# Kernel tuning notes

Hardware: AMD Instinct MI355X
Metric: run time of the kernel (lower is better)

The kernel has to match this reference:

```python
import jax, jax.numpy as jnp
import numpy as np

N_NODES = 100000
N_EDGES = 1600000
IN_C, HID_C, OUT_C = 128, 128, 64


def gcn_conv(x, src, dst, W, b, num_nodes):
    # PyG GCNConv: add self-loops, symmetric normalization, linear transform,
    # aggregate source features into targets.
    h = x @ W  # [N, C_out]
    loop = jnp.arange(num_nodes, dtype=src.dtype)
    s = jnp.concatenate([src, loop])
    d = jnp.concatenate([dst, loop])
    deg = jax.ops.segment_sum(jnp.ones_like(d, dtype=h.dtype), d, num_segments=num_nodes)
    inv_sqrt = jnp.where(deg > 0, jax.lax.rsqrt(deg), 0.0)
    norm = inv_sqrt[s] * inv_sqrt[d]  # [E+N]
    msgs = h[s] * norm[:, None]  # gather + scale
    out = jax.ops.segment_sum(msgs, d, num_segments=num_nodes)  # scatter-add
    return out + b


def setup_inputs() -> dict:
    key = jax.random.key(0)
    k1, k2, k3, k4 = jax.random.split(key, 4)
    x = jax.random.normal(k1, (N_NODES, IN_C), dtype=jnp.float32)
    edge_index = jax.random.randint(k2, (2, N_EDGES), 0, N_NODES, dtype=jnp.int64)
    W1 = jax.random.normal(k3, (IN_C, HID_C), dtype=jnp.float32) * (1.0 / np.sqrt(IN_C))
    b1 = jnp.zeros((HID_C,), dtype=jnp.float32)
    W2 = jax.random.normal(k4, (HID_C, OUT_C), dtype=jnp.float32) * (1.0 / np.sqrt(HID_C))
    b2 = jnp.zeros((OUT_C,), dtype=jnp.float32)
    return {"x": x, "edge_index": edge_index, "W1": W1, "b1": b1, "W2": W2, "b2": b2}


def reference(x, edge_index, W1, b1, W2, b2):
    num_nodes = x.shape[0]
    src, dst = edge_index[0], edge_index[1]  # PyG flow: source -> target
    h = gcn_conv(x, src, dst, W1, b1, num_nodes)
    h = jax.nn.relu(h)  # dropout is identity in eval mode
    out = gcn_conv(h, src, dst, W2, b2, num_nodes)
    return out
```

## Files before the change

kernel.cpp:

```cpp
#include <hip/hip_runtime.h>

#define IN_C 128
#define HID_C 128
#define OUT_C 64

#define BSPAN 256
#define BCAP  5120
#define NBMAX 512
#define ACHUNK 4096

typedef unsigned int uint32;
typedef unsigned short ushort16;
typedef _Float16 f16;
typedef f16   f16x8 __attribute__((ext_vector_type(8)));
typedef float f32x4 __attribute__((ext_vector_type(4)));


__device__ __forceinline__ ushort16 f2bf(float f) {
    union { float f; uint32 u; } v; v.f = f;
    uint32 r = v.u + 0x7FFFu + ((v.u >> 16) & 1u);
    return (ushort16)(r >> 16);
}

__device__ __forceinline__ void unpack2(uint32 u, float& f0, float& f1) {
    union { uint32 x; float f; } a, b;
    a.x = u << 16;
    b.x = u & 0xFFFF0000u;
    f0 = a.f; f1 = b.f;
}

__device__ __forceinline__ void acc_row(uint4 r, float* acc) {
    float f0, f1;
    unpack2(r.x, f0, f1); acc[0] += f0; acc[1] += f1;
    unpack2(r.y, f0, f1); acc[2] += f0; acc[3] += f1;
    unpack2(r.z, f0, f1); acc[4] += f0; acc[5] += f1;
    unpack2(r.w, f0, f1); acc[6] += f0; acc[7] += f1;
}


__launch_bounds__(256)
__global__ void bin_edges_kernel(const int* __restrict__ src, const int* __restrict__ dst,
                                 int* __restrict__ bucketCur, uint32* __restrict__ binned,
                                 int E, int nbuck) {
    __shared__ int hist[NBMAX];
    __shared__ int base[NBMAX];
    const int tid = threadIdx.x;
    const int e0  = blockIdx.x * ACHUNK;

    for (int i = tid; i < NBMAX; i += 256) hist[i] = 0;
    __syncthreads();

    int d[16], s[16], rk[16];
#pragma unroll
    for (int j = 0; j < 16; j++) {
        int e = e0 + j * 256 + tid;
        if (e < E) {
            d[j] = dst[e];
            s[j] = src[e];
            rk[j] = atomicAdd(&hist[d[j] >> 8], 1);
        } else d[j] = -1;
    }
    __syncthreads();

    for (int b = tid; b < nbuck; b += 256) {
        int h = hist[b];
        base[b] = h ? atomicAdd(&bucketCur[b], h) : 0;
    }
    __syncthreads();

#pragma unroll
    for (int j = 0; j < 16; j++) {
        if (d[j] >= 0) {
            int b = d[j] >> 8;
            int pos = base[b] + rk[j];
            if (pos < BCAP)
                binned[(size_t)b * BCAP + pos] =
                    ((uint32)(d[j] & 255) << 17) | (uint32)s[j];
        }
    }
}


__launch_bounds__(256)
__global__ void bucket_csr_kernel(const uint32* __restrict__ binned,
                                  const int* __restrict__ bucketCur,
                                  int* __restrict__ csr_src, int* __restrict__ rowbeg,
                                  int* __restrict__ rowend, float* __restrict__ inv, int N) {
    constexpr int MAXIT = BCAP / 256;
    __shared__ int cnt[BSPAN];
    __shared__ int scn[BSPAN];
    __shared__ int excl[BSPAN];
    const int b   = blockIdx.x;
    const int tid = threadIdx.x;
    const int n0  = b * BSPAN;
    const int ne  = min(bucketCur[b], BCAP);
    const uint32* bp = binned + (size_t)b * BCAP;

    cnt[tid] = 0;
    __syncthreads();

    uint32 ebuf[MAXIT];
    int    rbuf[MAXIT];
    int nmine = 0;
    for (int i = tid; i < ne; i += 256) {
        uint32 e = bp[i];
        ebuf[nmine] = e;
        rbuf[nmine] = atomicAdd(&cnt[e >> 17], 1);
        nmine++;
    }
    __syncthreads();

    int v = cnt[tid];
    scn[tid] = v;
    __syncthreads();
    for (int off = 1; off < 256; off <<= 1) {
        int u = (tid >= off) ? scn[tid - off] : 0;
        __syncthreads();
        scn[tid] += u;
        __syncthreads();
    }
    int ex = scn[tid] - v;
    excl[tid] = ex;

    int n = n0 + tid;
    if (n < N) {
        int gb = b * BCAP + ex;
        rowbeg[n] = gb;
        rowend[n] = gb + v;
        inv[n] = rsqrtf((float)(v + 1));
    }
    __syncthreads();

    for (int j = 0; j < nmine; j++) {
        uint32 e = ebuf[j];
        csr_src[(size_t)b * BCAP + excl[e >> 17] + rbuf[j]] = (int)(e & 0x1FFFFu);
    }
}


template <int C>
__device__ __forceinline__ void wprep_one(const float* __restrict__ W, f16* __restrict__ Wf, int t) {
    constexpr int NCT = C / 16;
    int lane = t & 63;
    int ctkc = t >> 6;
    int ct = ctkc % NCT, kc = ctkc / NCT;
    int kbase = kc * 32 + (lane >> 4) * 8;
    int col   = ct * 16 + (lane & 15);
    f16 v[8];
#pragma unroll
    for (int j = 0; j < 8; j++) v[j] = (f16)W[(size_t)(kbase + j) * C + col];
    *(uint4*)(Wf + (size_t)t * 8) = *(const uint4*)v;
}

__global__ void wprep_both(const float* __restrict__ W1, f16* __restrict__ Wf1,
                           const float* __restrict__ W2, f16* __restrict__ Wf2,
                           int* __restrict__ bucketCur, int nbuck) {
    constexpr int T1 = 4 * (HID_C / 16) * 64;
    constexpr int T2 = 4 * (OUT_C / 16) * 64;
    int t = blockIdx.x * 256 + threadIdx.x;
    if (t < nbuck) bucketCur[t] = 0;
    if (t < T1)            wprep_one<HID_C>(W1, Wf1, t);
    else if (t < T1 + T2)  wprep_one<OUT_C>(W2, Wf2, t - T1);
}


template <int C>
__launch_bounds__(256)
__global__ void mfma_gemm(const float* __restrict__ X, const f16* __restrict__ Wf,
                          const float* __restrict__ inv, ushort16* __restrict__ outb, int N) {
    constexpr int NCT = C / 16;
    __shared__ __align__(16) f16 As[4 * 4 * 64 * 8];
    __shared__ __align__(16) f16 Bs[4 * NCT * 64 * 8];

    const int tid  = threadIdx.x;
    const int lane = tid & 63;
    const int w    = tid >> 6;
    const int row0 = blockIdx.x * 64;

    {
        constexpr int TOT = 4 * NCT * 64 * 8;
        const uint4* src = (const uint4*)Wf;
        uint4* dst = (uint4*)Bs;
#pragma unroll
        for (int i = 0; i < TOT / 8 / 256; i++)
            dst[tid + i * 256] = src[tid + i * 256];
    }

    {
        int r   = tid >> 2;
        int seg = tid & 3;
        int row = row0 + r;
        int ws_ = r >> 4;
        int r15 = r & 15;
#pragma unroll
        for (int i = 0; i < 8; i++) {
            int k = seg * 32 + i * 4;
            float4 v = make_float4(0.f, 0.f, 0.f, 0.f);
            if (row < N) v = *(const float4*)(X + (size_t)row * 128 + k);
            int q = (k >> 3) & 3, j0 = k & 7;
            f16 h[4] = {(f16)v.x, (f16)v.y, (f16)v.z, (f16)v.w};
            int slot = ((seg * 4 + ws_) * 64 + (q * 16 + r15)) * 8 + j0;
            *(uint2*)(As + slot) = *(const uint2*)h;
        }
    }
    __syncthreads();

    f32x4 acc[NCT];
#pragma unroll
    for (int c = 0; c < NCT; c++) acc[c] = (f32x4){0.f, 0.f, 0.f, 0.f};
#pragma unroll
    for (int kc = 0; kc < 4; kc++) {
        f16x8 a = *(const f16x8*)&As[((kc * 4 + w) * 64 + lane) * 8];
#pragma unroll
        for (int ct = 0; ct < NCT; ct++) {
            f16x8 b = *(const f16x8*)&Bs[((kc * NCT + ct) * 64 + lane) * 8];
            acc[ct] = __builtin_amdgcn_mfma_f32_16x16x32_f16(a, b, acc[ct], 0, 0, 0);
        }
    }

    __syncthreads();
    ushort16* Ds = (ushort16*)As;
    const int q = lane >> 4;
    float iv[4];
#pragma unroll
    for (int reg = 0; reg < 4; reg++) {
        int row = row0 + w * 16 + q * 4 + reg;
        iv[reg] = (row < N) ? inv[row] : 0.f;
    }
#pragma unroll
    for (int ct = 0; ct < NCT; ct++) {
#pragma unroll
        for (int reg = 0; reg < 4; reg++) {
            int r = w * 16 + q * 4 + reg;
            Ds[r * C + ct * 16 + (lane & 15)] = f2bf(acc[ct][reg] * iv[reg]);
        }
    }
    __syncthreads();
    {
        int r  = tid >> 2;
        int row = row0 + r;
        if (row < N) {
            constexpr int SPT = C / 4;
            int c0 = (tid & 3) * SPT;
            const uint4* s = (const uint4*)&Ds[r * C + c0];
            uint4* d = (uint4*)(outb + (size_t)row * C + c0);
#pragma unroll
            for (int i = 0; i < SPT / 8; i++) d[i] = s[i];
        }
    }
}


__launch_bounds__(512, 4)
__global__ void fused_gather_gemm(const int* __restrict__ rowbeg, const int* __restrict__ rowend,
                                  const int* __restrict__ csr,
                                  const ushort16* __restrict__ hsb,
                                  const float* __restrict__ inv, const float* __restrict__ bias1,
                                  const f16* __restrict__ Wf2,
                                  ushort16* __restrict__ outb, int N) {
    constexpr int CIN = 128, COUT = 64, NCT = COUT / 16;
    __shared__ __align__(16) f16 As[4 * 4 * 64 * 8];
    __shared__ __align__(16) f16 Bs[4 * NCT * 64 * 8];

    const int tid  = threadIdx.x;
    const int lane = tid & 63;
    const int w    = tid >> 6;
    const int row0 = blockIdx.x * 64;

    {
        const uint4* s = (const uint4*)Wf2;
        uint4* d = (uint4*)Bs;
        d[tid]       = s[tid];
        d[tid + 512] = s[tid + 512];
    }

    {
        const int r = tid >> 3;
        const int q = tid & 7;
        const int n = row0 + r;
        float acc[16];
#pragma unroll
        for (int j = 0; j < 16; j++) acc[j] = 0.f;

        if (n < N) {
            {
                const ushort16* base = hsb + (size_t)n * CIN + q * 16;
                uint4 s0 = *(const uint4*)(base);
                uint4 s1 = *(const uint4*)(base + 8);
                acc_row(s0, acc); acc_row(s1, acc + 8);
            }
            const int end = rowend[n];
            int i = rowbeg[n];
            for (; i + 4 <= end; i += 4) {
                const ushort16* p0 = hsb + (size_t)csr[i]     * CIN + q * 16;
                const ushort16* p1 = hsb + (size_t)csr[i + 1] * CIN + q * 16;
                const ushort16* p2 = hsb + (size_t)csr[i + 2] * CIN + q * 16;
                const ushort16* p3 = hsb + (size_t)csr[i + 3] * CIN + q * 16;
                uint4 a0 = *(const uint4*)(p0);
                uint4 a1 = *(const uint4*)(p0 + 8);
                uint4 b0 = *(const uint4*)(p1);
                uint4 b1 = *(const uint4*)(p1 + 8);
                uint4 c0 = *(const uint4*)(p2);
                uint4 c1 = *(const uint4*)(p2 + 8);
                uint4 d0 = *(const uint4*)(p3);
                uint4 d1 = *(const uint4*)(p3 + 8);
                acc_row(a0, acc); acc_row(a1, acc + 8);
                acc_row(b0, acc); acc_row(b1, acc + 8);
                acc_row(c0, acc); acc_row(c1, acc + 8);
                acc_row(d0, acc); acc_row(d1, acc + 8);
            }
            for (; i < end; i++) {
                const ushort16* p0 = hsb + (size_t)csr[i] * CIN + q * 16;
                uint4 a0 = *(const uint4*)(p0);
                uint4 a1 = *(const uint4*)(p0 + 8);
                acc_row(a0, acc); acc_row(a1, acc + 8);
            }

            float iv = inv[n];
#pragma unroll
            for (int j = 0; j < 16; j++)
                acc[j] = fmaxf(fmaf(iv, acc[j], bias1[q * 16 + j]), 0.f);
        }

        const int ws_ = r >> 4, r15 = r & 15;
        const int seg = q >> 1;
#pragma unroll
        for (int u = 0; u < 2; u++) {
            const int i8 = (q & 1) * 2 + u;
            f16 hv[8];
#pragma unroll
            for (int j = 0; j < 8; j++) hv[j] = (f16)acc[u * 8 + j];
            int slot = ((seg * 4 + ws_) * 64 + (i8 * 16 + r15)) * 8;
            *(uint4*)(As + slot) = *(const uint4*)hv;
        }
    }
    __syncthreads();

    f32x4 acc2[NCT];
#pragma unroll
    for (int c = 0; c < NCT; c++) acc2[c] = (f32x4){0.f, 0.f, 0.f, 0.f};
    if (w < 4) {
#pragma unroll
        for (int kc = 0; kc < 4; kc++) {
            f16x8 a = *(const f16x8*)&As[((kc * 4 + w) * 64 + lane) * 8];
#pragma unroll
            for (int ct = 0; ct < NCT; ct++) {
                f16x8 b = *(const f16x8*)&Bs[((kc * NCT + ct) * 64 + lane) * 8];
                acc2[ct] = __builtin_amdgcn_mfma_f32_16x16x32_f16(a, b, acc2[ct], 0, 0, 0);
            }
        }
    }

    __syncthreads();
    ushort16* Ds = (ushort16*)As;
    if (w < 4) {
        const int q2 = lane >> 4;
        float iv2[4];
#pragma unroll
        for (int reg = 0; reg < 4; reg++) {
            int row = row0 + w * 16 + q2 * 4 + reg;
            iv2[reg] = (row < N) ? inv[row] : 0.f;
        }
#pragma unroll
        for (int ct = 0; ct < NCT; ct++) {
#pragma unroll
            for (int reg = 0; reg < 4; reg++) {
                int r = w * 16 + q2 * 4 + reg;
                Ds[r * COUT + ct * 16 + (lane & 15)] = f2bf(acc2[ct][reg] * iv2[reg]);
            }
        }
    }
    __syncthreads();
    {
        const int r   = tid >> 3;
        const int row = row0 + r;
        if (row < N) {
            const int c0 = (tid & 7) * 8;
            *(uint4*)(outb + (size_t)row * COUT + c0) = *(const uint4*)&Ds[r * COUT + c0];
        }
    }
}


template <int C, bool RELU>
__launch_bounds__(256, 4)
__global__ void gather_agg_bf16(const int* __restrict__ rowbeg, const int* __restrict__ rowend,
                                const int* __restrict__ csr_src,
                                const ushort16* __restrict__ hsb, const float* __restrict__ inv,
                                const float* __restrict__ b, float* __restrict__ out, int N) {
    constexpr int TPN = 4;
    constexpr int CPT = C / TPN;
    constexpr int NPB = 256 / TPN;
    int n    = blockIdx.x * NPB + threadIdx.x / TPN;
    int lane = threadIdx.x % TPN;
    if (n >= N) return;
    const size_t c0 = (size_t)lane * CPT;

    float acc[16];
#pragma unroll
    for (int j = 0; j < 16; j++) acc[j] = 0.f;
    {
        const uint4* p = (const uint4*)(hsb + (size_t)n * C + c0);
        uint4 s0 = p[0], s1 = p[1];
        acc_row(s0, acc); acc_row(s1, acc + 8);
    }

    const int end = rowend[n];
    int i = rowbeg[n];
    for (; i + 4 <= end; i += 4) {
        const uint4* p0 = (const uint4*)(hsb + (size_t)csr_src[i]     * C + c0);
        const uint4* p1 = (const uint4*)(hsb + (size_t)csr_src[i + 1] * C + c0);
        const uint4* p2 = (const uint4*)(hsb + (size_t)csr_src[i + 2] * C + c0);
        const uint4* p3 = (const uint4*)(hsb + (size_t)csr_src[i + 3] * C + c0);
        uint4 a0 = p0[0], a1 = p0[1];
        uint4 b0 = p1[0], b1 = p1[1];
        uint4 cc0 = p2[0], cc1 = p2[1];
        uint4 d0 = p3[0], d1 = p3[1];
        acc_row(a0, acc);  acc_row(a1, acc + 8);
        acc_row(b0, acc);  acc_row(b1, acc + 8);
        acc_row(cc0, acc); acc_row(cc1, acc + 8);
        acc_row(d0, acc);  acc_row(d1, acc + 8);
    }
    for (; i < end; i++) {
        const uint4* p0 = (const uint4*)(hsb + (size_t)csr_src[i] * C + c0);
        uint4 a0 = p0[0], a1 = p0[1];
        acc_row(a0, acc); acc_row(a1, acc + 8);
    }

    float iv = inv[n];
    float r[16];
#pragma unroll
    for (int u = 0; u < 4; u++) {
        float4 bv = *(const float4*)(b + c0 + u * 4);
        r[u * 4 + 0] = fmaf(iv, acc[u * 4 + 0], bv.x);
        r[u * 4 + 1] = fmaf(iv, acc[u * 4 + 1], bv.y);
        r[u * 4 + 2] = fmaf(iv, acc[u * 4 + 2], bv.z);
        r[u * 4 + 3] = fmaf(iv, acc[u * 4 + 3], bv.w);
    }
    if (RELU) {
#pragma unroll
        for (int j = 0; j < 16; j++) r[j] = fmaxf(r[j], 0.f);
    }
    float* po = out + (size_t)n * C + c0;
#pragma unroll
    for (int u = 0; u < 4; u++)
        *(float4*)(po + u * 4) = make_float4(r[u * 4 + 0], r[u * 4 + 1], r[u * 4 + 2], r[u * 4 + 3]);
}

extern "C" void kernel_launch(void* const* d_in, const int* in_sizes, int n_in,
                              void* d_out, int out_size, void* d_ws, size_t ws_size,
                              hipStream_t stream) {
    const float* x  = (const float*)d_in[0];
    const int*   ei = (const int*)d_in[1];
    const float* W1 = (const float*)d_in[2];
    const float* b1 = (const float*)d_in[3];
    const float* W2 = (const float*)d_in[4];
    const float* b2 = (const float*)d_in[5];
    float* out = (float*)d_out;

    const int N = in_sizes[0] / IN_C;
    const int E = in_sizes[1] / 2;
    const int* src = ei;
    const int* dst = ei + E;
    const int nbuck = (N + BSPAN - 1) / BSPAN;

    char* ws = (char*)d_ws;
    auto align_up = [](size_t v) { return (v + 1023) & ~(size_t)1023; };
    size_t off = 0;
    int*      bucketCur = (int*)(ws + off);      off += align_up((size_t)nbuck * sizeof(int));
    float*    inv       = (float*)(ws + off);    off += align_up((size_t)N * sizeof(float));
    int*      rowbeg    = (int*)(ws + off);      off += align_up((size_t)N * sizeof(int));
    int*      rowend    = (int*)(ws + off);      off += align_up((size_t)N * sizeof(int));
    uint32*   binned    = (uint32*)(ws + off);   off += align_up((size_t)nbuck * BCAP * sizeof(uint32));
    int*      csrs      = (int*)(ws + off);      off += align_up((size_t)nbuck * BCAP * sizeof(int));
    f16*      Wf1       = (f16*)(ws + off);      off += align_up((size_t)4 * (HID_C/16) * 64 * 8 * sizeof(f16));
    f16*      Wf2       = (f16*)(ws + off);      off += align_up((size_t)4 * (OUT_C/16) * 64 * 8 * sizeof(f16));
    ushort16* hs1b      = (ushort16*)(ws + off); off += align_up((size_t)N * HID_C * sizeof(ushort16));
    ushort16* hs2b      = (ushort16*)(ws + off); off += align_up((size_t)N * OUT_C * sizeof(ushort16));

    wprep_both<<<(4 * (HID_C/16 + OUT_C/16) * 64 + 255) / 256, 256, 0, stream>>>(
        W1, Wf1, W2, Wf2, bucketCur, nbuck);
    bin_edges_kernel<<<(E + ACHUNK - 1) / ACHUNK, 256, 0, stream>>>(
        src, dst, bucketCur, binned, E, nbuck);
    bucket_csr_kernel<<<nbuck, 256, 0, stream>>>(
        binned, bucketCur, csrs, rowbeg, rowend, inv, N);

    mfma_gemm<HID_C><<<(N + 63) / 64, 256, 0, stream>>>(x, Wf1, inv, hs1b, N);

    fused_gather_gemm<<<(N + 63) / 64, 512, 0, stream>>>(
        rowbeg, rowend, csrs, hs1b, inv, b1, Wf2, hs2b, N);

    gather_agg_bf16<OUT_C, false><<<(N + 63) / 64, 256, 0, stream>>>(
        rowbeg, rowend, csrs, hs2b, inv, b2, out, N);
}
```

Measured before the change: 263.2 us.

## Store layer-2 features as fp16 column slices and gather per slice

```diff
diff --git a/kernel.cpp b/kernel.cpp
--- a/kernel.cpp
+++ b/kernel.cpp
@@ -257,7 +257,7 @@
                                   const ushort16* __restrict__ hsb,
                                   const float* __restrict__ inv, const float* __restrict__ bias1,
                                   const f16* __restrict__ Wf2,
-                                  ushort16* __restrict__ outb, int N) {
+                                  f16* __restrict__ hs2s, int N) {
     constexpr int CIN = 128, COUT = 64, NCT = COUT / 16;
     __shared__ __align__(16) f16 As[4 * 4 * 64 * 8];
     __shared__ __align__(16) f16 Bs[4 * NCT * 64 * 8];
@@ -352,7 +352,7 @@
     }
 
     __syncthreads();
-    ushort16* Ds = (ushort16*)As;
+    f16* Ds = (f16*)As;
     if (w < 4) {
         const int q2 = lane >> 4;
         float iv2[4];
@@ -366,7 +366,7 @@
 #pragma unroll
             for (int reg = 0; reg < 4; reg++) {
                 int r = w * 16 + q2 * 4 + reg;
-                Ds[r * COUT + ct * 16 + (lane & 15)] = f2bf(acc2[ct][reg] * iv2[reg]);
+                Ds[r * COUT + ct * 16 + (lane & 15)] = (f16)(acc2[ct][reg] * iv2[reg]);
             }
         }
     }
@@ -375,76 +375,67 @@
         const int r   = tid >> 3;
         const int row = row0 + r;
         if (row < N) {
-            const int c0 = (tid & 7) * 8;
-            *(uint4*)(outb + (size_t)row * COUT + c0) = *(const uint4*)&Ds[r * COUT + c0];
-        }
-    }
-}
-
-
-template <int C, bool RELU>
-__launch_bounds__(256, 4)
-__global__ void gather_agg_bf16(const int* __restrict__ rowbeg, const int* __restrict__ rowend,
-                                const int* __restrict__ csr_src,
-                                const ushort16* __restrict__ hsb, const float* __restrict__ inv,
-                                const float* __restrict__ b, float* __restrict__ out, int N) {
-    constexpr int TPN = 4;
-    constexpr int CPT = C / TPN;
-    constexpr int NPB = 256 / TPN;
-    int n    = blockIdx.x * NPB + threadIdx.x / TPN;
-    int lane = threadIdx.x % TPN;
+            const int c = tid & 7;
+            const int s = c >> 1, h = c & 1;
+            uint4 v = *(const uint4*)&Ds[r * COUT + c * 8];
+            *(uint4*)(hs2s + ((size_t)s * N + row) * 16 + h * 8) = v;
+        }
+    }
+}
+
+
+__launch_bounds__(256)
+__global__ void slice_gather2(const int* __restrict__ rowbeg, const int* __restrict__ rowend,
+                              const int* __restrict__ csr_src,
+                              const f16* __restrict__ hs2s,
+                              const float* __restrict__ inv, const float* __restrict__ b,
+                              float* __restrict__ out, int N) {
+    const int s = blockIdx.x & 3;
+    const int n = (blockIdx.x >> 2) * 256 + threadIdx.x;
     if (n >= N) return;
-    const size_t c0 = (size_t)lane * CPT;
+    const f16* base = hs2s + (size_t)s * N * 16;
 
     float acc[16];
-#pragma unroll
-    for (int j = 0; j < 16; j++) acc[j] = 0.f;
-    {
-        const uint4* p = (const uint4*)(hsb + (size_t)n * C + c0);
-        uint4 s0 = p[0], s1 = p[1];
-        acc_row(s0, acc); acc_row(s1, acc + 8);
+    {
+        const f16x8* p = (const f16x8*)(base + (size_t)n * 16);
+        f16x8 a0 = p[0], a1 = p[1];
+#pragma unroll
+        for (int j = 0; j < 8; j++) { acc[j] = (float)a0[j]; acc[8 + j] = (float)a1[j]; }
     }
 
     const int end = rowend[n];
     int i = rowbeg[n];
     for (; i + 4 <= end; i += 4) {
-        const uint4* p0 = (const uint4*)(hsb + (size_t)csr_src[i]     * C + c0);
-        const uint4* p1 = (const uint4*)(hsb + (size_t)csr_src[i + 1] * C + c0);
-        const uint4* p2 = (const uint4*)(hsb + (size_t)csr_src[i + 2] * C + c0);
-        const uint4* p3 = (const uint4*)(hsb + (size_t)csr_src[i + 3] * C + c0);
-        uint4 a0 = p0[0], a1 = p0[1];
-        uint4 b0 = p1[0], b1 = p1[1];
-        uint4 cc0 = p2[0], cc1 = p2[1];
-        uint4 d0 = p3[0], d1 = p3[1];
-        acc_row(a0, acc);  acc_row(a1, acc + 8);
-        acc_row(b0, acc);  acc_row(b1, acc + 8);
-        acc_row(cc0, acc); acc_row(cc1, acc + 8);
-        acc_row(d0, acc);  acc_row(d1, acc + 8);
+        const f16x8* p0 = (const f16x8*)(base + (size_t)csr_src[i]     * 16);
+        const f16x8* p1 = (const f16x8*)(base + (size_t)csr_src[i + 1] * 16);
+        const f16x8* p2 = (const f16x8*)(base + (size_t)csr_src[i + 2] * 16);
+        const f16x8* p3 = (const f16x8*)(base + (size_t)csr_src[i + 3] * 16);
+        f16x8 a0 = p0[0], a1 = p0[1];
+        f16x8 b0 = p1[0], b1 = p1[1];
+        f16x8 c0 = p2[0], c1 = p2[1];
+        f16x8 d0 = p3[0], d1 = p3[1];
+#pragma unroll
+        for (int j = 0; j < 8; j++) {
+            acc[j]     += (float)a0[j] + (float)b0[j] + (float)c0[j] + (float)d0[j];
+            acc[8 + j] += (float)a1[j] + (float)b1[j] + (float)c1[j] + (float)d1[j];
+        }
     }
     for (; i < end; i++) {
-        const uint4* p0 = (const uint4*)(hsb + (size_t)csr_src[i] * C + c0);
-        uint4 a0 = p0[0], a1 = p0[1];
-        acc_row(a0, acc); acc_row(a1, acc + 8);
-    }
-
-    float iv = inv[n];
-    float r[16];
-#pragma unroll
-    for (int u = 0; u < 4; u++) {
-        float4 bv = *(const float4*)(b + c0 + u * 4);
-        r[u * 4 + 0] = fmaf(iv, acc[u * 4 + 0], bv.x);
-        r[u * 4 + 1] = fmaf(iv, acc[u * 4 + 1], bv.y);
-        r[u * 4 + 2] = fmaf(iv, acc[u * 4 + 2], bv.z);
-        r[u * 4 + 3] = fmaf(iv, acc[u * 4 + 3], bv.w);
-    }
-    if (RELU) {
-#pragma unroll
-        for (int j = 0; j < 16; j++) r[j] = fmaxf(r[j], 0.f);
-    }
-    float* po = out + (size_t)n * C + c0;
+        const f16x8* p0 = (const f16x8*)(base + (size_t)csr_src[i] * 16);
+        f16x8 a0 = p0[0], a1 = p0[1];
+#pragma unroll
+        for (int j = 0; j < 8; j++) { acc[j] += (float)a0[j]; acc[8 + j] += (float)a1[j]; }
+    }
+
+    const float iv = inv[n];
+    const float* bp = b + s * 16;
+    float* po = out + (size_t)n * 64 + s * 16;
+#pragma unroll
+    for (int j = 0; j < 16; j++) acc[j] = fmaf(iv, acc[j], bp[j]);
 #pragma unroll
     for (int u = 0; u < 4; u++)
-        *(float4*)(po + u * 4) = make_float4(r[u * 4 + 0], r[u * 4 + 1], r[u * 4 + 2], r[u * 4 + 3]);
+        *(float4*)(po + u * 4) = make_float4(acc[u * 4], acc[u * 4 + 1],
+                                             acc[u * 4 + 2], acc[u * 4 + 3]);
 }
 
 extern "C" void kernel_launch(void* const* d_in, const int* in_sizes, int n_in,
@@ -476,7 +467,7 @@
     f16*      Wf1       = (f16*)(ws + off);      off += align_up((size_t)4 * (HID_C/16) * 64 * 8 * sizeof(f16));
     f16*      Wf2       = (f16*)(ws + off);      off += align_up((size_t)4 * (OUT_C/16) * 64 * 8 * sizeof(f16));
     ushort16* hs1b      = (ushort16*)(ws + off); off += align_up((size_t)N * HID_C * sizeof(ushort16));
-    ushort16* hs2b      = (ushort16*)(ws + off); off += align_up((size_t)N * OUT_C * sizeof(ushort16));
+    f16*      hs2s      = (f16*)(ws + off);      off += align_up((size_t)4 * N * 16 * sizeof(f16));
 
     wprep_both<<<(4 * (HID_C/16 + OUT_C/16) * 64 + 255) / 256, 256, 0, stream>>>(
         W1, Wf1, W2, Wf2, bucketCur, nbuck);
@@ -488,8 +479,8 @@
     mfma_gemm<HID_C><<<(N + 63) / 64, 256, 0, stream>>>(x, Wf1, inv, hs1b, N);
 
     fused_gather_gemm<<<(N + 63) / 64, 512, 0, stream>>>(
-        rowbeg, rowend, csrs, hs1b, inv, b1, Wf2, hs2b, N);
-
-    gather_agg_bf16<OUT_C, false><<<(N + 63) / 64, 256, 0, stream>>>(
-        rowbeg, rowend, csrs, hs2b, inv, b2, out, N);
-}
+        rowbeg, rowend, csrs, hs1b, inv, b1, Wf2, hs2s, N);
+
+    slice_gather2<<<((N + 255) / 256) * 4, 256, 0, stream>>>(
+        rowbeg, rowend, csrs, hs2s, inv, b2, out, N);
+}
```

Result: slower. 303.4 us (+15.3%).
